# Kernel tuning notes

Measured on AMD Instinct MI355X. Metric: run time of the kernel, lower is better.

The kernel has to match this reference:

```python
import jax, jax.numpy as jnp
import numpy as np

T, B, IN, OUT, N_MOD, K = 1024, 8, 1024, 1024, 16, 2

def setup_inputs() -> dict:
    key = jax.random.key(0)
    k1, k2, k3, k4 = jax.random.split(key, 4)
    x = jax.random.normal(k1, (T, B, IN), dtype=jnp.float32)
    selection = jax.random.randint(k2, (B, K), 0, N_MOD, dtype=jnp.int64)
    weight = jax.random.normal(k3, (N_MOD, IN, OUT), dtype=jnp.float32) * (1.0 / np.sqrt(IN))
    bias = jax.random.normal(k4, (N_MOD, OUT), dtype=jnp.float32) * 0.02
    return {"x": x, "selection": selection, "weight": weight, "bias": bias}

def reference(x, selection, weight, bias):
    # time_major=True: x is [T, B, in] -> batch-major [B, T, in]
    xb = jnp.swapaxes(x, 0, 1)
    # Gather the K selected expert weight matrices per batch row: [B, K, in, out]
    W_sel = weight[selection]
    # Equivalent to matmul(x[i], cat(weight[sel], dim=1)): [B, T, K, out]
    o = jnp.einsum('bti,bkio->btko', xb, W_sel)
    Bn, Tn, Kn, On = o.shape
    o = o.reshape(Bn, Tn, Kn * On)
    # concat_dim == 1 bias: bias[sel].view(1, -1) -> [1, K*out], broadcast over T
    o = o + bias[selection].reshape(Bn, 1, Kn * On)
    # back to time-major [T, B, K*out]
    return jnp.swapaxes(o, 0, 1)
```

## Files before the change

kernel.cpp:

```cpp
#include <hip/hip_runtime.h>

#define T_DIM 1024
#define B_DIM 8
#define IN_DIM 1024
#define OUT_DIM 1024
#define N_MODL 16
#define K_SEL 2

typedef unsigned short ushort_t;
typedef __bf16 bf16x8 __attribute__((ext_vector_type(8)));
typedef float f32x4 __attribute__((ext_vector_type(4)));

__device__ __forceinline__ unsigned int f2bf2(float lo, float hi) {
  union { float f; unsigned int u; } a, b; a.f = lo; b.f = hi;
  unsigned int ra = (a.u + 0x7fffu + ((a.u >> 16) & 1u)) >> 16;
  unsigned int rb = (b.u + 0x7fffu + ((b.u >> 16) & 1u)) >> 16;
  return ra | (rb << 16);
}

__device__ __forceinline__ void async_g2l(const void* g, void* l) {
  __builtin_amdgcn_global_load_lds(
      (const __attribute__((address_space(1))) unsigned int*)g,
      (__attribute__((address_space(3))) unsigned int*)l,
      16, 0, 0);
}

__device__ __forceinline__ int read_sel(const int* __restrict__ s, int g) {
  bool i64 = true;
#pragma unroll
  for (int j = 0; j < 8; ++j) i64 &= (s[2 * j + 1] == 0);
  return i64 ? s[2 * g] : s[g];
}

__global__ __launch_bounds__(256) void convert_kernel(const float* __restrict__ x,
                                                      const float* __restrict__ w,
                                                      const int* __restrict__ selp,
                                                      ushort_t* __restrict__ xb,
                                                      ushort_t* __restrict__ wt) {
  __shared__ ushort_t tb[128 * 128];
  const int bid = blockIdx.x;
  if (bid >= 1024) {
    const int i = (bid - 1024) * 256 + threadIdx.x;
    const float4* s = (const float4*)x;
    float4 a = s[i * 2], b = s[i * 2 + 1];
    uint4 o;
    o.x = f2bf2(a.x, a.y); o.y = f2bf2(a.z, a.w);
    o.z = f2bf2(b.x, b.y); o.w = f2bf2(b.z, b.w);
    ((uint4*)xb)[i] = o;
    return;
  }
  const int m = bid >> 6;
  bool used = false;
#pragma unroll
  for (int g = 0; g < B_DIM * K_SEL; ++g) used |= (read_sel(selp, g) == m);
  if (!used) return;

  const int i0 = ((bid >> 3) & 7) * 128;
  const int o0 = (bid & 7) * 128;
  const float* src = w + ((size_t)(m * IN_DIM + i0)) * OUT_DIM + o0;

  const int o4 = (threadIdx.x & 31) * 4;
  const int ib = threadIdx.x >> 5;
#pragma unroll
  for (int p = 0; p < 16; ++p) {
    const int i = ib + p * 8;
    float4 v = *(const float4*)(src + (size_t)i * OUT_DIM + o4);
    const int osw = o4 ^ (((i >> 3) & 15) << 2);
    uint2 d2; d2.x = f2bf2(v.x, v.y); d2.y = f2bf2(v.z, v.w);
    *(uint2*)(tb + i * 128 + osw) = d2;
  }
  __syncthreads();

  ushort_t* dst = wt + ((size_t)(m * OUT_DIM + o0)) * IN_DIM + i0;
  const int il = (threadIdx.x & 15) * 8;
  const int ob = threadIdx.x >> 4;
  const int q2 = ((il >> 3) & 15) << 2;
#pragma unroll
  for (int p = 0; p < 8; ++p) {
    const int o = ob + p * 16;
    const int osw = o ^ q2;
    uint4 d;
    unsigned int u[8];
#pragma unroll
    for (int j = 0; j < 8; ++j) u[j] = tb[(il + j) * 128 + osw];
    d.x = u[0] | (u[1] << 16); d.y = u[2] | (u[3] << 16);
    d.z = u[4] | (u[5] << 16); d.w = u[6] | (u[7] << 16);
    *(uint4*)(dst + (size_t)o * IN_DIM + il) = d;
  }
}

#define MFMA16 __builtin_amdgcn_mfma_f32_16x16x32_bf16

template<bool LAST>
__device__ __forceinline__ void gstep(
    int t, ushort_t* As,
    const ushort_t* curB0, const ushort_t* curB1,
    ushort_t* nxtB0, ushort_t* nxtB1,
    const ushort_t* Ab, const ushort_t* Bb0, const ushort_t* Bb1,
    int wv, int ardo, int brdo, int cb,
    f32x4 (&acc0)[4][4], f32x4 (&acc1)[4][4]) {
  const int k1 = (t + 1) * 64;
  if (!LAST) {
#pragma unroll
    for (int c = 0; c < 4; ++c) {
      const int j = wv * 4 + c;
      async_g2l(Bb0 + (size_t)8 * j * IN_DIM + k1, nxtB0 + j * 512);
      async_g2l(Bb1 + (size_t)8 * j * IN_DIM + k1, nxtB1 + j * 512);
    }
    __builtin_amdgcn_sched_barrier(0);
  }
  bf16x8 af0[4], af1[4];
  const ushort_t* Ard = As + ardo;
#pragma unroll
  for (int i = 0; i < 4; ++i) {
    af0[i] = *(const bf16x8*)(Ard + i * 1024 + cb);
    af1[i] = *(const bf16x8*)(Ard + i * 1024 + (cb ^ 32));
  }
  if (!LAST) {
    __builtin_amdgcn_sched_barrier(0);
    asm volatile("s_waitcnt lgkmcnt(0)" ::: "memory");
    __builtin_amdgcn_sched_barrier(0);
    __builtin_amdgcn_s_barrier();
    __builtin_amdgcn_sched_barrier(0);
#pragma unroll
    for (int c = 0; c < 4; ++c) {
      const int j = wv * 4 + c;
      async_g2l(Ab + (size_t)8 * j * (B_DIM * IN_DIM) + k1, As + j * 512);
    }
    __builtin_amdgcn_sched_barrier(0);
  }
  const ushort_t* Brd0 = curB0 + brdo;
  const ushort_t* Brd1 = curB1 + brdo;
  bf16x8 b0[4], b1[4];
#pragma unroll
  for (int n = 0; n < 4; ++n) {
    b0[n] = *(const bf16x8*)(Brd0 + n * 1024 + cb);
    b1[n] = *(const bf16x8*)(Brd1 + n * 1024 + cb);
  }
#pragma unroll
  for (int mt = 0; mt < 4; ++mt)
#pragma unroll
    for (int nt = 0; nt < 4; ++nt) {
      acc0[mt][nt] = MFMA16(af0[mt], b0[nt], acc0[mt][nt], 0, 0, 0);
      acc1[mt][nt] = MFMA16(af0[mt], b1[nt], acc1[mt][nt], 0, 0, 0);
    }
#pragma unroll
  for (int n = 0; n < 4; ++n) {
    b0[n] = *(const bf16x8*)(Brd0 + n * 1024 + (cb ^ 32));
    b1[n] = *(const bf16x8*)(Brd1 + n * 1024 + (cb ^ 32));
  }
#pragma unroll
  for (int mt = 0; mt < 4; ++mt)
#pragma unroll
    for (int nt = 0; nt < 4; ++nt) {
      acc0[mt][nt] = MFMA16(af1[mt], b0[nt], acc0[mt][nt], 0, 0, 0);
      acc1[mt][nt] = MFMA16(af1[mt], b1[nt], acc1[mt][nt], 0, 0, 0);
    }
  if (!LAST) {
    __builtin_amdgcn_sched_barrier(0);
    asm volatile("s_waitcnt vmcnt(0)" ::: "memory");
    __builtin_amdgcn_sched_barrier(0);
    __builtin_amdgcn_s_barrier();
    __builtin_amdgcn_sched_barrier(0);
  }
}

__global__ __launch_bounds__(256, 2) void mlgemm_kernel(const ushort_t* __restrict__ xb,
                                                        const ushort_t* __restrict__ wt,
                                                        const int* __restrict__ selp,
                                                        const float* __restrict__ bias,
                                                        float* __restrict__ out) {
  __shared__ ushort_t As[128 * 64];
  __shared__ ushort_t Bs[2][2][128 * 64];

  const int lin = blockIdx.x;
  const int b = lin & 7;
  const int mtile = (lin >> 3) & 7;
  const int ntile = lin >> 6;
  const int e0 = read_sel(selp, 2 * b);
  const int e1 = read_sel(selp, 2 * b + 1);
  const int m0 = mtile * 128;
  const int n0 = ntile * 128;

  const int lane = threadIdx.x & 63;
  const int wv = threadIdx.x >> 6;

  const int srow = lane >> 3;
  const int sx = (((lane & 7) ^ (srow & 7)) << 3);
  const ushort_t* Ab  = xb + (size_t)(m0 + srow) * (B_DIM * IN_DIM) + b * IN_DIM + sx;
  const ushort_t* Bb0 = wt + ((size_t)(e0 * OUT_DIM + n0 + srow)) * IN_DIM + sx;
  const ushort_t* Bb1 = wt + ((size_t)(e1 * OUT_DIM + n0 + srow)) * IN_DIM + sx;

  const int frow = lane & 15;
  const int quad = lane >> 4;
  const int cb = ((quad ^ (frow & 7)) << 3);
  const int wrow = (wv & 1) * 64;
  const int wcol = (wv >> 1) * 64;
  const int ardo = (wrow + frow) * 64;
  const int brdo = (wcol + frow) * 64;

  f32x4 acc0[4][4] = {};
  f32x4 acc1[4][4] = {};

#pragma unroll
  for (int c = 0; c < 4; ++c) {
    const int j = wv * 4 + c;
    async_g2l(Ab  + (size_t)8 * j * (B_DIM * IN_DIM), As + j * 512);
    async_g2l(Bb0 + (size_t)8 * j * IN_DIM, Bs[0][0] + j * 512);
    async_g2l(Bb1 + (size_t)8 * j * IN_DIM, Bs[0][1] + j * 512);
  }
  __builtin_amdgcn_sched_barrier(0);
  asm volatile("s_waitcnt vmcnt(0)" ::: "memory");
  __builtin_amdgcn_sched_barrier(0);
  __builtin_amdgcn_s_barrier();
  __builtin_amdgcn_sched_barrier(0);

  for (int t = 0; t < 14; t += 2) {
    gstep<false>(t,     As, Bs[0][0], Bs[0][1], Bs[1][0], Bs[1][1],
                 Ab, Bb0, Bb1, wv, ardo, brdo, cb, acc0, acc1);
    gstep<false>(t + 1, As, Bs[1][0], Bs[1][1], Bs[0][0], Bs[0][1],
                 Ab, Bb0, Bb1, wv, ardo, brdo, cb, acc0, acc1);
  }
  gstep<false>(14, As, Bs[0][0], Bs[0][1], Bs[1][0], Bs[1][1],
               Ab, Bb0, Bb1, wv, ardo, brdo, cb, acc0, acc1);
  gstep<true>(15, As, Bs[1][0], Bs[1][1], Bs[0][0], Bs[0][1],
              Ab, Bb0, Bb1, wv, ardo, brdo, cb, acc0, acc1);

  const int orow0 = m0 + wrow + quad * 4;
  const int ocol0 = n0 + wcol + frow;
  const float* bp0 = bias + (size_t)e0 * OUT_DIM;
  const float* bp1 = bias + (size_t)e1 * OUT_DIM;
  float bv0[4], bv1[4];
#pragma unroll
  for (int nt = 0; nt < 4; ++nt) {
    bv0[nt] = bp0[ocol0 + nt * 16];
    bv1[nt] = bp1[ocol0 + nt * 16];
  }
  float* C0 = out + (size_t)b * (K_SEL * OUT_DIM);
  float* C1 = C0 + OUT_DIM;
#pragma unroll
  for (int mt = 0; mt < 4; ++mt) {
#pragma unroll
    for (int r = 0; r < 4; ++r) {
      const size_t rowoff = (size_t)(orow0 + mt * 16 + r) * (B_DIM * K_SEL * OUT_DIM);
#pragma unroll
      for (int nt = 0; nt < 4; ++nt) {
        C0[rowoff + ocol0 + nt * 16] = acc0[mt][nt][r] + bv0[nt];
        C1[rowoff + ocol0 + nt * 16] = acc1[mt][nt][r] + bv1[nt];
      }
    }
  }
}

extern "C" void kernel_launch(void* const* d_in, const int* in_sizes, int n_in,
                              void* d_out, int out_size, void* d_ws, size_t ws_size,
                              hipStream_t stream) {
  const float* x    = (const float*)d_in[0];
  const int*   sel  = (const int*)d_in[1];
  const float* w    = (const float*)d_in[2];
  const float* bias = (const float*)d_in[3];
  float* out = (float*)d_out;

  ushort_t* xb = (ushort_t*)d_ws;
  ushort_t* wt = (ushort_t*)((char*)d_ws +
                             (size_t)T_DIM * B_DIM * IN_DIM * 2);

  convert_kernel<<<dim3(1024 + T_DIM * B_DIM * IN_DIM / 8 / 256), 256, 0, stream>>>(
      x, w, sel, xb, wt);
  mlgemm_kernel<<<dim3(8 * 8 * B_DIM), 256, 0, stream>>>(xb, wt, sel, bias, out);
}
```

Before: 174.8 us.

## Double M tile to 256 rows and double-buffer A tile in LDS

```diff
diff --git a/kernel.cpp b/kernel.cpp
--- a/kernel.cpp
+++ b/kernel.cpp
@@ -93,14 +93,18 @@
 
 template<bool LAST>
 __device__ __forceinline__ void gstep(
-    int t, ushort_t* As,
-    const ushort_t* curB0, const ushort_t* curB1,
-    ushort_t* nxtB0, ushort_t* nxtB1,
+    int t, const ushort_t* curA, const ushort_t* curB0, const ushort_t* curB1,
+    ushort_t* nxtA, ushort_t* nxtB0, ushort_t* nxtB1,
     const ushort_t* Ab, const ushort_t* Bb0, const ushort_t* Bb1,
     int wv, int ardo, int brdo, int cb,
-    f32x4 (&acc0)[4][4], f32x4 (&acc1)[4][4]) {
+    f32x4 (&acc0)[8][4], f32x4 (&acc1)[8][4]) {
   const int k1 = (t + 1) * 64;
   if (!LAST) {
+#pragma unroll
+    for (int c = 0; c < 8; ++c) {
+      const int j = wv * 8 + c;
+      async_g2l(Ab + (size_t)8 * j * (B_DIM * IN_DIM) + k1, nxtA + j * 512);
+    }
 #pragma unroll
     for (int c = 0; c < 4; ++c) {
       const int j = wv * 4 + c;
@@ -109,53 +113,28 @@
     }
     __builtin_amdgcn_sched_barrier(0);
   }
-  bf16x8 af0[4], af1[4];
-  const ushort_t* Ard = As + ardo;
-#pragma unroll
-  for (int i = 0; i < 4; ++i) {
-    af0[i] = *(const bf16x8*)(Ard + i * 1024 + cb);
-    af1[i] = *(const bf16x8*)(Ard + i * 1024 + (cb ^ 32));
-  }
-  if (!LAST) {
-    __builtin_amdgcn_sched_barrier(0);
-    asm volatile("s_waitcnt lgkmcnt(0)" ::: "memory");
-    __builtin_amdgcn_sched_barrier(0);
-    __builtin_amdgcn_s_barrier();
-    __builtin_amdgcn_sched_barrier(0);
-#pragma unroll
-    for (int c = 0; c < 4; ++c) {
-      const int j = wv * 4 + c;
-      async_g2l(Ab + (size_t)8 * j * (B_DIM * IN_DIM) + k1, As + j * 512);
-    }
-    __builtin_amdgcn_sched_barrier(0);
-  }
+  const ushort_t* Ard  = curA + ardo;
   const ushort_t* Brd0 = curB0 + brdo;
   const ushort_t* Brd1 = curB1 + brdo;
-  bf16x8 b0[4], b1[4];
-#pragma unroll
-  for (int n = 0; n < 4; ++n) {
-    b0[n] = *(const bf16x8*)(Brd0 + n * 1024 + cb);
-    b1[n] = *(const bf16x8*)(Brd1 + n * 1024 + cb);
-  }
-#pragma unroll
-  for (int mt = 0; mt < 4; ++mt)
-#pragma unroll
-    for (int nt = 0; nt < 4; ++nt) {
-      acc0[mt][nt] = MFMA16(af0[mt], b0[nt], acc0[mt][nt], 0, 0, 0);
-      acc1[mt][nt] = MFMA16(af0[mt], b1[nt], acc1[mt][nt], 0, 0, 0);
-    }
-#pragma unroll
-  for (int n = 0; n < 4; ++n) {
-    b0[n] = *(const bf16x8*)(Brd0 + n * 1024 + (cb ^ 32));
-    b1[n] = *(const bf16x8*)(Brd1 + n * 1024 + (cb ^ 32));
-  }
-#pragma unroll
-  for (int mt = 0; mt < 4; ++mt)
-#pragma unroll
-    for (int nt = 0; nt < 4; ++nt) {
-      acc0[mt][nt] = MFMA16(af1[mt], b0[nt], acc0[mt][nt], 0, 0, 0);
-      acc1[mt][nt] = MFMA16(af1[mt], b1[nt], acc1[mt][nt], 0, 0, 0);
-    }
+#pragma unroll
+  for (int kk = 0; kk < 2; ++kk) {
+    const int co = kk ? (cb ^ 32) : cb;
+    bf16x8 af[8], b0[4], b1[4];
+#pragma unroll
+    for (int i = 0; i < 8; ++i) af[i] = *(const bf16x8*)(Ard + i * 1024 + co);
+#pragma unroll
+    for (int n = 0; n < 4; ++n) {
+      b0[n] = *(const bf16x8*)(Brd0 + n * 1024 + co);
+      b1[n] = *(const bf16x8*)(Brd1 + n * 1024 + co);
+    }
+#pragma unroll
+    for (int mt = 0; mt < 8; ++mt)
+#pragma unroll
+      for (int nt = 0; nt < 4; ++nt) {
+        acc0[mt][nt] = MFMA16(af[mt], b0[nt], acc0[mt][nt], 0, 0, 0);
+        acc1[mt][nt] = MFMA16(af[mt], b1[nt], acc1[mt][nt], 0, 0, 0);
+      }
+  }
   if (!LAST) {
     __builtin_amdgcn_sched_barrier(0);
     asm volatile("s_waitcnt vmcnt(0)" ::: "memory");
@@ -165,21 +144,21 @@
   }
 }
 
-__global__ __launch_bounds__(256, 2) void mlgemm_kernel(const ushort_t* __restrict__ xb,
+__global__ __launch_bounds__(256, 1) void mlgemm_kernel(const ushort_t* __restrict__ xb,
                                                         const ushort_t* __restrict__ wt,
                                                         const int* __restrict__ selp,
                                                         const float* __restrict__ bias,
                                                         float* __restrict__ out) {
-  __shared__ ushort_t As[128 * 64];
+  __shared__ ushort_t As[2][256 * 64];
   __shared__ ushort_t Bs[2][2][128 * 64];
 
   const int lin = blockIdx.x;
   const int b = lin & 7;
-  const int mtile = (lin >> 3) & 7;
-  const int ntile = lin >> 6;
+  const int mtile = (lin >> 3) & 3;
+  const int ntile = lin >> 5;
   const int e0 = read_sel(selp, 2 * b);
   const int e1 = read_sel(selp, 2 * b + 1);
-  const int m0 = mtile * 128;
+  const int m0 = mtile * 256;
   const int n0 = ntile * 128;
 
   const int lane = threadIdx.x & 63;
@@ -194,18 +173,22 @@
   const int frow = lane & 15;
   const int quad = lane >> 4;
   const int cb = ((quad ^ (frow & 7)) << 3);
-  const int wrow = (wv & 1) * 64;
+  const int wrow = (wv & 1) * 128;
   const int wcol = (wv >> 1) * 64;
   const int ardo = (wrow + frow) * 64;
   const int brdo = (wcol + frow) * 64;
 
-  f32x4 acc0[4][4] = {};
-  f32x4 acc1[4][4] = {};
-
+  f32x4 acc0[8][4] = {};
+  f32x4 acc1[8][4] = {};
+
+#pragma unroll
+  for (int c = 0; c < 8; ++c) {
+    const int j = wv * 8 + c;
+    async_g2l(Ab + (size_t)8 * j * (B_DIM * IN_DIM), As[0] + j * 512);
+  }
 #pragma unroll
   for (int c = 0; c < 4; ++c) {
     const int j = wv * 4 + c;
-    async_g2l(Ab  + (size_t)8 * j * (B_DIM * IN_DIM), As + j * 512);
     async_g2l(Bb0 + (size_t)8 * j * IN_DIM, Bs[0][0] + j * 512);
     async_g2l(Bb1 + (size_t)8 * j * IN_DIM, Bs[0][1] + j * 512);
   }
@@ -216,14 +199,14 @@
   __builtin_amdgcn_sched_barrier(0);
 
   for (int t = 0; t < 14; t += 2) {
-    gstep<false>(t,     As, Bs[0][0], Bs[0][1], Bs[1][0], Bs[1][1],
+    gstep<false>(t,     As[0], Bs[0][0], Bs[0][1], As[1], Bs[1][0], Bs[1][1],
                  Ab, Bb0, Bb1, wv, ardo, brdo, cb, acc0, acc1);
-    gstep<false>(t + 1, As, Bs[1][0], Bs[1][1], Bs[0][0], Bs[0][1],
+    gstep<false>(t + 1, As[1], Bs[1][0], Bs[1][1], As[0], Bs[0][0], Bs[0][1],
                  Ab, Bb0, Bb1, wv, ardo, brdo, cb, acc0, acc1);
   }
-  gstep<false>(14, As, Bs[0][0], Bs[0][1], Bs[1][0], Bs[1][1],
+  gstep<false>(14, As[0], Bs[0][0], Bs[0][1], As[1], Bs[1][0], Bs[1][1],
                Ab, Bb0, Bb1, wv, ardo, brdo, cb, acc0, acc1);
-  gstep<true>(15, As, Bs[1][0], Bs[1][1], Bs[0][0], Bs[0][1],
+  gstep<true>(15, As[1], Bs[1][0], Bs[1][1], As[0], Bs[0][0], Bs[0][1],
               Ab, Bb0, Bb1, wv, ardo, brdo, cb, acc0, acc1);
 
   const int orow0 = m0 + wrow + quad * 4;
@@ -239,7 +222,7 @@
   float* C0 = out + (size_t)b * (K_SEL * OUT_DIM);
   float* C1 = C0 + OUT_DIM;
 #pragma unroll
-  for (int mt = 0; mt < 4; ++mt) {
+  for (int mt = 0; mt < 8; ++mt) {
 #pragma unroll
     for (int r = 0; r < 4; ++r) {
       const size_t rowoff = (size_t)(orow0 + mt * 16 + r) * (B_DIM * K_SEL * OUT_DIM);
@@ -267,5 +250,5 @@
 
   convert_kernel<<<dim3(1024 + T_DIM * B_DIM * IN_DIM / 8 / 256), 256, 0, stream>>>(
       x, w, sel, xb, wt);
-  mlgemm_kernel<<<dim3(8 * 8 * B_DIM), 256, 0, stream>>>(xb, wt, sel, bias, out);
-}
+  mlgemm_kernel<<<dim3(8 * 4 * 8), 256, 0, stream>>>(xb, wt, sel, bias, out);
+}
```

After: 187.7 us. +7.4%, slower.

## Load A fragments directly from global memory instead of staging through LDS

Applied to the files above, without the earlier changes.

```diff
diff --git a/kernel.cpp b/kernel.cpp
--- a/kernel.cpp
+++ b/kernel.cpp
@@ -93,14 +93,22 @@
 
 template<bool LAST>
 __device__ __forceinline__ void gstep(
-    int t, ushort_t* As,
-    const ushort_t* curB0, const ushort_t* curB1,
+    int t, const ushort_t* curB0, const ushort_t* curB1,
     ushort_t* nxtB0, ushort_t* nxtB1,
-    const ushort_t* Ab, const ushort_t* Bb0, const ushort_t* Bb1,
-    int wv, int ardo, int brdo, int cb,
+    const ushort_t* Ag, const ushort_t* Bb0, const ushort_t* Bb1,
+    int wv, int brdo, int cb,
     f32x4 (&acc0)[4][4], f32x4 (&acc1)[4][4]) {
-  const int k1 = (t + 1) * 64;
+  const int k0 = t * 64;
+  bf16x8 af0[4], af1[4];
+#pragma unroll
+  for (int i = 0; i < 4; ++i) {
+    const ushort_t* ap = Ag + (size_t)i * 16 * (B_DIM * IN_DIM) + k0;
+    af0[i] = *(const bf16x8*)(ap);
+    af1[i] = *(const bf16x8*)(ap + 32);
+  }
+  __builtin_amdgcn_sched_barrier(0);
   if (!LAST) {
+    const int k1 = k0 + 64;
 #pragma unroll
     for (int c = 0; c < 4; ++c) {
       const int j = wv * 4 + c;
@@ -109,53 +117,26 @@
     }
     __builtin_amdgcn_sched_barrier(0);
   }
-  bf16x8 af0[4], af1[4];
-  const ushort_t* Ard = As + ardo;
-#pragma unroll
-  for (int i = 0; i < 4; ++i) {
-    af0[i] = *(const bf16x8*)(Ard + i * 1024 + cb);
-    af1[i] = *(const bf16x8*)(Ard + i * 1024 + (cb ^ 32));
-  }
-  if (!LAST) {
-    __builtin_amdgcn_sched_barrier(0);
-    asm volatile("s_waitcnt lgkmcnt(0)" ::: "memory");
-    __builtin_amdgcn_sched_barrier(0);
-    __builtin_amdgcn_s_barrier();
-    __builtin_amdgcn_sched_barrier(0);
-#pragma unroll
-    for (int c = 0; c < 4; ++c) {
-      const int j = wv * 4 + c;
-      async_g2l(Ab + (size_t)8 * j * (B_DIM * IN_DIM) + k1, As + j * 512);
-    }
-    __builtin_amdgcn_sched_barrier(0);
-  }
   const ushort_t* Brd0 = curB0 + brdo;
   const ushort_t* Brd1 = curB1 + brdo;
-  bf16x8 b0[4], b1[4];
-#pragma unroll
-  for (int n = 0; n < 4; ++n) {
-    b0[n] = *(const bf16x8*)(Brd0 + n * 1024 + cb);
-    b1[n] = *(const bf16x8*)(Brd1 + n * 1024 + cb);
-  }
-#pragma unroll
-  for (int mt = 0; mt < 4; ++mt)
-#pragma unroll
-    for (int nt = 0; nt < 4; ++nt) {
-      acc0[mt][nt] = MFMA16(af0[mt], b0[nt], acc0[mt][nt], 0, 0, 0);
-      acc1[mt][nt] = MFMA16(af0[mt], b1[nt], acc1[mt][nt], 0, 0, 0);
+#pragma unroll
+  for (int kk = 0; kk < 2; ++kk) {
+    const int co = kk ? (cb ^ 32) : cb;
+    bf16x8 b0[4], b1[4];
+#pragma unroll
+    for (int n = 0; n < 4; ++n) {
+      b0[n] = *(const bf16x8*)(Brd0 + n * 1024 + co);
+      b1[n] = *(const bf16x8*)(Brd1 + n * 1024 + co);
     }
-#pragma unroll
-  for (int n = 0; n < 4; ++n) {
-    b0[n] = *(const bf16x8*)(Brd0 + n * 1024 + (cb ^ 32));
-    b1[n] = *(const bf16x8*)(Brd1 + n * 1024 + (cb ^ 32));
-  }
-#pragma unroll
-  for (int mt = 0; mt < 4; ++mt)
-#pragma unroll
-    for (int nt = 0; nt < 4; ++nt) {
-      acc0[mt][nt] = MFMA16(af1[mt], b0[nt], acc0[mt][nt], 0, 0, 0);
-      acc1[mt][nt] = MFMA16(af1[mt], b1[nt], acc1[mt][nt], 0, 0, 0);
-    }
+    const bf16x8* afp = kk ? af1 : af0;
+#pragma unroll
+    for (int mt = 0; mt < 4; ++mt)
+#pragma unroll
+      for (int nt = 0; nt < 4; ++nt) {
+        acc0[mt][nt] = MFMA16(afp[mt], b0[nt], acc0[mt][nt], 0, 0, 0);
+        acc1[mt][nt] = MFMA16(afp[mt], b1[nt], acc1[mt][nt], 0, 0, 0);
+      }
+  }
   if (!LAST) {
     __builtin_amdgcn_sched_barrier(0);
     asm volatile("s_waitcnt vmcnt(0)" ::: "memory");
@@ -170,7 +151,6 @@
                                                         const int* __restrict__ selp,
                                                         const float* __restrict__ bias,
                                                         float* __restrict__ out) {
-  __shared__ ushort_t As[128 * 64];
   __shared__ ushort_t Bs[2][2][128 * 64];
 
   const int lin = blockIdx.x;
@@ -187,7 +167,6 @@
 
   const int srow = lane >> 3;
   const int sx = (((lane & 7) ^ (srow & 7)) << 3);
-  const ushort_t* Ab  = xb + (size_t)(m0 + srow) * (B_DIM * IN_DIM) + b * IN_DIM + sx;
   const ushort_t* Bb0 = wt + ((size_t)(e0 * OUT_DIM + n0 + srow)) * IN_DIM + sx;
   const ushort_t* Bb1 = wt + ((size_t)(e1 * OUT_DIM + n0 + srow)) * IN_DIM + sx;
 
@@ -196,8 +175,10 @@
   const int cb = ((quad ^ (frow & 7)) << 3);
   const int wrow = (wv & 1) * 64;
   const int wcol = (wv >> 1) * 64;
-  const int ardo = (wrow + frow) * 64;
   const int brdo = (wcol + frow) * 64;
+
+  const ushort_t* Ag = xb + (size_t)(m0 + wrow + frow) * (B_DIM * IN_DIM)
+                          + b * IN_DIM + quad * 8;
 
   f32x4 acc0[4][4] = {};
   f32x4 acc1[4][4] = {};
@@ -205,7 +186,6 @@
 #pragma unroll
   for (int c = 0; c < 4; ++c) {
     const int j = wv * 4 + c;
-    async_g2l(Ab  + (size_t)8 * j * (B_DIM * IN_DIM), As + j * 512);
     async_g2l(Bb0 + (size_t)8 * j * IN_DIM, Bs[0][0] + j * 512);
     async_g2l(Bb1 + (size_t)8 * j * IN_DIM, Bs[0][1] + j * 512);
   }
@@ -216,15 +196,15 @@
   __builtin_amdgcn_sched_barrier(0);
 
   for (int t = 0; t < 14; t += 2) {
-    gstep<false>(t,     As, Bs[0][0], Bs[0][1], Bs[1][0], Bs[1][1],
-                 Ab, Bb0, Bb1, wv, ardo, brdo, cb, acc0, acc1);
-    gstep<false>(t + 1, As, Bs[1][0], Bs[1][1], Bs[0][0], Bs[0][1],
-                 Ab, Bb0, Bb1, wv, ardo, brdo, cb, acc0, acc1);
-  }
-  gstep<false>(14, As, Bs[0][0], Bs[0][1], Bs[1][0], Bs[1][1],
-               Ab, Bb0, Bb1, wv, ardo, brdo, cb, acc0, acc1);
-  gstep<true>(15, As, Bs[1][0], Bs[1][1], Bs[0][0], Bs[0][1],
-              Ab, Bb0, Bb1, wv, ardo, brdo, cb, acc0, acc1);
+    gstep<false>(t,     Bs[0][0], Bs[0][1], Bs[1][0], Bs[1][1],
+                 Ag, Bb0, Bb1, wv, brdo, cb, acc0, acc1);
+    gstep<false>(t + 1, Bs[1][0], Bs[1][1], Bs[0][0], Bs[0][1],
+                 Ag, Bb0, Bb1, wv, brdo, cb, acc0, acc1);
+  }
+  gstep<false>(14, Bs[0][0], Bs[0][1], Bs[1][0], Bs[1][1],
+               Ag, Bb0, Bb1, wv, brdo, cb, acc0, acc1);
+  gstep<true>(15, Bs[1][0], Bs[1][1], Bs[0][0], Bs[0][1],
+              Ag, Bb0, Bb1, wv, brdo, cb, acc0, acc1);
 
   const int orow0 = m0 + wrow + quad * 4;
   const int ocol0 = n0 + wcol + frow;
```

After: 189.1 us. 8.2% more time.

## Stage GEMM epilogue through LDS for coalesced float4 stores; raise MFMA wave priority

Applied to the files above, without the earlier changes.

```diff
diff --git a/kernel.cpp b/kernel.cpp
--- a/kernel.cpp
+++ b/kernel.cpp
@@ -137,6 +137,7 @@
     b0[n] = *(const bf16x8*)(Brd0 + n * 1024 + cb);
     b1[n] = *(const bf16x8*)(Brd1 + n * 1024 + cb);
   }
+  __builtin_amdgcn_s_setprio(1);
 #pragma unroll
   for (int mt = 0; mt < 4; ++mt)
 #pragma unroll
@@ -144,11 +145,13 @@
       acc0[mt][nt] = MFMA16(af0[mt], b0[nt], acc0[mt][nt], 0, 0, 0);
       acc1[mt][nt] = MFMA16(af0[mt], b1[nt], acc1[mt][nt], 0, 0, 0);
     }
+  __builtin_amdgcn_s_setprio(0);
 #pragma unroll
   for (int n = 0; n < 4; ++n) {
     b0[n] = *(const bf16x8*)(Brd0 + n * 1024 + (cb ^ 32));
     b1[n] = *(const bf16x8*)(Brd1 + n * 1024 + (cb ^ 32));
   }
+  __builtin_amdgcn_s_setprio(1);
 #pragma unroll
   for (int mt = 0; mt < 4; ++mt)
 #pragma unroll
@@ -156,6 +159,7 @@
       acc0[mt][nt] = MFMA16(af1[mt], b0[nt], acc0[mt][nt], 0, 0, 0);
       acc1[mt][nt] = MFMA16(af1[mt], b1[nt], acc1[mt][nt], 0, 0, 0);
     }
+  __builtin_amdgcn_s_setprio(0);
   if (!LAST) {
     __builtin_amdgcn_sched_barrier(0);
     asm volatile("s_waitcnt vmcnt(0)" ::: "memory");
@@ -170,8 +174,9 @@
                                                         const int* __restrict__ selp,
                                                         const float* __restrict__ bias,
                                                         float* __restrict__ out) {
-  __shared__ ushort_t As[128 * 64];
-  __shared__ ushort_t Bs[2][2][128 * 64];
+  __shared__ __align__(16) ushort_t smem[40960];
+  ushort_t* As = smem;
+#define BSP(buf, e) (smem + 8192 + ((buf) * 2 + (e)) * 8192)
 
   const int lin = blockIdx.x;
   const int b = lin & 7;
@@ -182,8 +187,9 @@
   const int m0 = mtile * 128;
   const int n0 = ntile * 128;
 
-  const int lane = threadIdx.x & 63;
-  const int wv = threadIdx.x >> 6;
+  const int tid = threadIdx.x;
+  const int lane = tid & 63;
+  const int wv = tid >> 6;
 
   const int srow = lane >> 3;
   const int sx = (((lane & 7) ^ (srow & 7)) << 3);
@@ -206,8 +212,8 @@
   for (int c = 0; c < 4; ++c) {
     const int j = wv * 4 + c;
     async_g2l(Ab  + (size_t)8 * j * (B_DIM * IN_DIM), As + j * 512);
-    async_g2l(Bb0 + (size_t)8 * j * IN_DIM, Bs[0][0] + j * 512);
-    async_g2l(Bb1 + (size_t)8 * j * IN_DIM, Bs[0][1] + j * 512);
+    async_g2l(Bb0 + (size_t)8 * j * IN_DIM, BSP(0, 0) + j * 512);
+    async_g2l(Bb1 + (size_t)8 * j * IN_DIM, BSP(0, 1) + j * 512);
   }
   __builtin_amdgcn_sched_barrier(0);
   asm volatile("s_waitcnt vmcnt(0)" ::: "memory");
@@ -216,40 +222,63 @@
   __builtin_amdgcn_sched_barrier(0);
 
   for (int t = 0; t < 14; t += 2) {
-    gstep<false>(t,     As, Bs[0][0], Bs[0][1], Bs[1][0], Bs[1][1],
+    gstep<false>(t,     As, BSP(0, 0), BSP(0, 1), BSP(1, 0), BSP(1, 1),
                  Ab, Bb0, Bb1, wv, ardo, brdo, cb, acc0, acc1);
-    gstep<false>(t + 1, As, Bs[1][0], Bs[1][1], Bs[0][0], Bs[0][1],
+    gstep<false>(t + 1, As, BSP(1, 0), BSP(1, 1), BSP(0, 0), BSP(0, 1),
                  Ab, Bb0, Bb1, wv, ardo, brdo, cb, acc0, acc1);
   }
-  gstep<false>(14, As, Bs[0][0], Bs[0][1], Bs[1][0], Bs[1][1],
+  gstep<false>(14, As, BSP(0, 0), BSP(0, 1), BSP(1, 0), BSP(1, 1),
                Ab, Bb0, Bb1, wv, ardo, brdo, cb, acc0, acc1);
-  gstep<true>(15, As, Bs[1][0], Bs[1][1], Bs[0][0], Bs[0][1],
+  gstep<true>(15, As, BSP(1, 0), BSP(1, 1), BSP(0, 0), BSP(0, 1),
               Ab, Bb0, Bb1, wv, ardo, brdo, cb, acc0, acc1);
 
-  const int orow0 = m0 + wrow + quad * 4;
-  const int ocol0 = n0 + wcol + frow;
+  __syncthreads();
+
+  float* fb = (float*)smem;
   const float* bp0 = bias + (size_t)e0 * OUT_DIM;
   const float* bp1 = bias + (size_t)e1 * OUT_DIM;
+  const int ocol0 = n0 + wcol + frow;
   float bv0[4], bv1[4];
 #pragma unroll
   for (int nt = 0; nt < 4; ++nt) {
     bv0[nt] = bp0[ocol0 + nt * 16];
     bv1[nt] = bp1[ocol0 + nt * 16];
   }
-  float* C0 = out + (size_t)b * (K_SEL * OUT_DIM);
-  float* C1 = C0 + OUT_DIM;
-#pragma unroll
-  for (int mt = 0; mt < 4; ++mt) {
-#pragma unroll
-    for (int r = 0; r < 4; ++r) {
-      const size_t rowoff = (size_t)(orow0 + mt * 16 + r) * (B_DIM * K_SEL * OUT_DIM);
-#pragma unroll
-      for (int nt = 0; nt < 4; ++nt) {
-        C0[rowoff + ocol0 + nt * 16] = acc0[mt][nt][r] + bv0[nt];
-        C1[rowoff + ocol0 + nt * 16] = acc1[mt][nt][r] + bv1[nt];
-      }
-    }
-  }
+
+#pragma unroll
+  for (int r = 0; r < 2; ++r) {
+    if ((wv & 1) == r) {
+#pragma unroll
+      for (int mt = 0; mt < 4; ++mt)
+#pragma unroll
+        for (int rr = 0; rr < 4; ++rr) {
+          const int rowl = mt * 16 + quad * 4 + rr;
+#pragma unroll
+          for (int nt = 0; nt < 4; ++nt) {
+            const int col = wcol + frow + nt * 16;
+            fb[rowl * 260 + col]       = acc0[mt][nt][rr] + bv0[nt];
+            fb[rowl * 260 + 128 + col] = acc1[mt][nt][rr] + bv1[nt];
+          }
+        }
+    }
+    __syncthreads();
+    const int rl_base = tid >> 5;
+    const int lir = tid & 31;
+#pragma unroll
+    for (int p = 0; p < 16; ++p) {
+      const int e = p >> 3;
+      const int rowl = (p & 7) * 8 + rl_base;
+      const float* s = fb + rowl * 260 + e * 128 + lir * 4;
+      float4 v = *(const float4*)s;
+      const int grow = m0 + r * 64 + rowl;
+      float* d = out + (size_t)grow * (B_DIM * K_SEL * OUT_DIM)
+                     + (size_t)b * (K_SEL * OUT_DIM)
+                     + (size_t)e * OUT_DIM + n0 + lir * 4;
+      *(float4*)d = v;
+    }
+    __syncthreads();
+  }
+#undef BSP
 }
 
 extern "C" void kernel_launch(void* const* d_in, const int* in_sizes, int n_in,
```

Result: no change. 174.9 us (+0.1%).
